# Optimization experiments

Hardware: AMD Instinct MI355X
Metric: run time of the kernel (lower is better)

Reference implementation:

```python
import jax, jax.numpy as jnp
import numpy as np

T = 12      # time_steps
N = 10000   # nodes per timestep graph
E = 160000  # edges per timestep graph
P = 30000   # node pairs
DIN = 128   # input_dim
H = 64      # hidden_dim
WND = 4     # attn_wnd


def setup_inputs() -> dict:
    key = jax.random.key(0)
    ks = jax.random.split(key, 12)
    x = jax.random.normal(ks[0], (2, T, N, DIN), dtype=jnp.float32)
    src = jax.random.randint(ks[1], (2, T, E), 0, N, dtype=jnp.int32)
    dst = jax.random.randint(ks[2], (2, T, E), 0, N, dtype=jnp.int32)
    idx = jax.random.randint(ks[3], (2, T, P), 0, N, dtype=jnp.int32)
    w_self = jax.random.normal(ks[4], (DIN, H), dtype=jnp.float32) * (1.0 / np.sqrt(DIN))
    w_neigh = jax.random.normal(ks[5], (DIN, H), dtype=jnp.float32) * (1.0 / np.sqrt(DIN))
    b_sage = jnp.zeros((H,), jnp.float32)
    w_ff2 = jax.random.normal(ks[6], (2 * H,), dtype=jnp.float32) * (1.0 / np.sqrt(2 * H))
    b_ff2 = jnp.zeros((), jnp.float32)
    w_ff1 = jax.random.normal(ks[7], (T,), dtype=jnp.float32) * (1.0 / np.sqrt(T))
    b_ff1 = jnp.zeros((), jnp.float32)
    w_out = jax.random.normal(ks[8], (2 * H, 1), dtype=jnp.float32) * (1.0 / np.sqrt(2 * H))
    return dict(x=x, src=src, dst=dst, idx=idx, w_self=w_self, w_neigh=w_neigh,
                b_sage=b_sage, w_ff2=w_ff2, b_ff2=b_ff2, w_ff1=w_ff1, b_ff1=b_ff1,
                w_out=w_out)


def _sage_all(x, src, dst, w_self, w_neigh, b_sage):
    """Mean-aggregation SAGEConv + L2 normalize, run over all 2*T graphs via scan."""
    xs = (x.reshape(2 * T, N, DIN), src.reshape(2 * T, E), dst.reshape(2 * T, E))

    def step(_, xe):
        xt, s, d = xe
        msum = jax.ops.segment_sum(xt[s], d, num_segments=N)            # [N, DIN]
        deg = jax.ops.segment_sum(jnp.ones((E,), xt.dtype), d, num_segments=N)
        mean = msum / jnp.maximum(deg, 1.0)[:, None]
        h = xt @ w_self + mean @ w_neigh + b_sage                       # [N, H]
        h = h / jnp.maximum(jnp.linalg.norm(h, axis=1, keepdims=True), 1e-12)
        return None, h

    _, hs = jax.lax.scan(step, None, xs)
    return hs.reshape(2, T, N, H)


def reference(x, src, dst, idx, w_self, w_neigh, b_sage, w_ff2, b_ff2, w_ff1, b_ff1, w_out):
    h = _sage_all(x, src, dst, w_self, w_neigh, b_sage)                 # [2, T, N, H]
    t_ar = jnp.arange(T)[:, None]
    hi = h[0][t_ar, idx[0]]                                             # [T, P, H]
    hj = h[1][t_ar, idx[1]]                                             # [T, P, H]
    temporal = jnp.concatenate([hi, hj], axis=-1).transpose(1, 0, 2)    # [P, T, 2H]

    def shifted(k):  # zero-pad shift along time by k
        return jnp.concatenate([jnp.zeros_like(temporal[:, :k]), temporal[:, :-k]], axis=1)

    # diff[k] = temporal - temporal shifted by (k+1) steps, k in [0, WND-2]
    diffs = jnp.stack([temporal - shifted(k + 1) for k in range(WND - 1)])  # [W-1, P, T, 2H]
    dw = jax.nn.relu(diffs @ w_ff2 + b_ff2)                              # [W-1, P, T]
    s = dw @ w_ff1 + b_ff1                                               # [W-1, P]
    sw = jax.nn.softmax(s, axis=0)[:, :, None, None]                     # softmax over window axis
    diff_att = jnp.sum(sw * jax.nn.sigmoid(diffs), axis=0)               # [P, T, 2H]
    outs = (temporal * diff_att).transpose(1, 0, 2)                      # [T, P, 2H]
    return (outs @ w_out)[..., 0]                                        # [T, P]
```

## Files before the change

kernel.cpp:

```cpp
#include <hip/hip_runtime.h>
#include <hip/hip_bf16.h>

#define TT 12
#define NNODE 10000
#define NEDGE 160000
#define NPAIR 30000
#define DIN 128
#define HH 64
#define NG 24
#define NROWS (NG * NNODE)
#define NEALL (NG * NEDGE)

typedef __attribute__((ext_vector_type(8))) short short8v;
typedef __attribute__((ext_vector_type(4))) float f32x4;

__device__ __forceinline__ short f2bf(float f) {
    unsigned u = __float_as_uint(f);
    unsigned r = u + 0x7fffu + ((u >> 16) & 1u);
    return (short)(r >> 16);
}
__device__ __forceinline__ float bf2f(short s) {
    return __uint_as_float(((unsigned)(unsigned short)s) << 16);
}

__global__ __launch_bounds__(256) void k_gemm_n(const float* __restrict__ x,
                                                const float* __restrict__ w,
                                                float* __restrict__ xn) {
    const int l = threadIdx.x & 63;
    const int wv = threadIdx.x >> 6;
    const int base = blockIdx.x * 64 + wv * 16;
    const int r15 = l & 15, q = l >> 4;
    f32x4 acc[4];
    #pragma unroll
    for (int c = 0; c < 4; ++c) acc[c] = (f32x4)0.f;
    #pragma unroll
    for (int s = 0; s < 4; ++s) {
        const float* xr = x + (size_t)(base + r15) * DIN + s * 32 + q * 8;
        float4 a0 = *(const float4*)xr;
        float4 a1 = *(const float4*)(xr + 4);
        float av[8] = {a0.x, a0.y, a0.z, a0.w, a1.x, a1.y, a1.z, a1.w};
        short8v ah, al;
        #pragma unroll
        for (int j = 0; j < 8; ++j) {
            short h = f2bf(av[j]); ah[j] = h; al[j] = f2bf(av[j] - bf2f(h));
        }
        #pragma unroll
        for (int c = 0; c < 4; ++c) {
            const float* wp = w + (size_t)(s * 32 + q * 8) * HH + c * 16 + r15;
            short8v bh, bl;
            #pragma unroll
            for (int j = 0; j < 8; ++j) {
                float v = wp[(size_t)j * HH];
                short h = f2bf(v); bh[j] = h; bl[j] = f2bf(v - bf2f(h));
            }
            acc[c] = __builtin_amdgcn_mfma_f32_16x16x32_bf16(ah, bh, acc[c], 0, 0, 0);
            acc[c] = __builtin_amdgcn_mfma_f32_16x16x32_bf16(ah, bl, acc[c], 0, 0, 0);
            acc[c] = __builtin_amdgcn_mfma_f32_16x16x32_bf16(al, bh, acc[c], 0, 0, 0);
        }
    }
    #pragma unroll
    for (int c = 0; c < 4; ++c)
        #pragma unroll
        for (int r = 0; r < 4; ++r)
            xn[(size_t)(base + q * 4 + r) * HH + c * 16 + r15] = acc[c][r];
}

__global__ __launch_bounds__(256) void k_gemm_sfin(const float* __restrict__ x,
                                                   const float* __restrict__ w,
                                                   const float* __restrict__ b_sage,
                                                   const float* __restrict__ msum,
                                                   float* __restrict__ hout) {
    const int l = threadIdx.x & 63;
    const int wv = threadIdx.x >> 6;
    const int base = blockIdx.x * 64 + wv * 16;
    const int r15 = l & 15, q = l >> 4;
    f32x4 acc[4];
    #pragma unroll
    for (int c = 0; c < 4; ++c) acc[c] = (f32x4)0.f;
    #pragma unroll
    for (int s = 0; s < 4; ++s) {
        const float* xr = x + (size_t)(base + r15) * DIN + s * 32 + q * 8;
        float4 a0 = *(const float4*)xr;
        float4 a1 = *(const float4*)(xr + 4);
        float av[8] = {a0.x, a0.y, a0.z, a0.w, a1.x, a1.y, a1.z, a1.w};
        short8v ah, al;
        #pragma unroll
        for (int j = 0; j < 8; ++j) {
            short h = f2bf(av[j]); ah[j] = h; al[j] = f2bf(av[j] - bf2f(h));
        }
        #pragma unroll
        for (int c = 0; c < 4; ++c) {
            const float* wp = w + (size_t)(s * 32 + q * 8) * HH + c * 16 + r15;
            short8v bh, bl;
            #pragma unroll
            for (int j = 0; j < 8; ++j) {
                float v = wp[(size_t)j * HH];
                short h = f2bf(v); bh[j] = h; bl[j] = f2bf(v - bf2f(h));
            }
            acc[c] = __builtin_amdgcn_mfma_f32_16x16x32_bf16(ah, bh, acc[c], 0, 0, 0);
            acc[c] = __builtin_amdgcn_mfma_f32_16x16x32_bf16(ah, bl, acc[c], 0, 0, 0);
            acc[c] = __builtin_amdgcn_mfma_f32_16x16x32_bf16(al, bh, acc[c], 0, 0, 0);
        }
    }
    float val[4][4];
    #pragma unroll
    for (int c = 0; c < 4; ++c) {
        int col = c * 16 + r15;
        float bb = b_sage[col];
        #pragma unroll
        for (int r = 0; r < 4; ++r) {
            int row = base + q * 4 + r;
            val[c][r] = acc[c][r] + bb + msum[(size_t)row * HH + col];
        }
    }
    #pragma unroll
    for (int r = 0; r < 4; ++r) {
        float ss = val[0][r] * val[0][r] + val[1][r] * val[1][r] +
                   val[2][r] * val[2][r] + val[3][r] * val[3][r];
        #pragma unroll
        for (int off = 1; off < 16; off <<= 1) ss += __shfl_xor(ss, off);
        float nrm = sqrtf(ss);
        nrm = nrm > 1e-12f ? nrm : 1e-12f;
        float inv = 1.f / nrm;
        #pragma unroll
        for (int c = 0; c < 4; ++c)
            hout[(size_t)(base + q * 4 + r) * HH + c * 16 + r15] = val[c][r] * inv;
    }
}

__global__ __launch_bounds__(256) void k_hist(const int* __restrict__ dst,
                                              int* __restrict__ deg_i) {
    int e = blockIdx.x * 256 + threadIdx.x;
    if (e >= NEALL) return;
    int g = e / NEDGE;
    atomicAdd(&deg_i[g * NNODE + dst[e]], 1);
}

__global__ __launch_bounds__(256) void k_scan(const int* __restrict__ deg_i,
                                              int* __restrict__ cursor) {
    const int g = blockIdx.x;
    const int t = threadIdx.x;
    const int base = g * NNODE;
    const int start = t * 40;
    const int cnt = start < NNODE ? (NNODE - start < 40 ? NNODE - start : 40) : 0;
    int s = 0;
    for (int i = 0; i < cnt; ++i) s += deg_i[base + start + i];
    __shared__ int sb[256];
    sb[t] = s;
    __syncthreads();
    #pragma unroll
    for (int d = 1; d < 256; d <<= 1) {
        int v = (t >= d) ? sb[t - d] : 0;
        __syncthreads();
        sb[t] += v;
        __syncthreads();
    }
    int run = sb[t] - s;
    for (int i = 0; i < cnt; ++i) {
        int d = deg_i[base + start + i];
        cursor[base + start + i] = run;
        run += d;
    }
}

__global__ __launch_bounds__(256) void k_fill(const int* __restrict__ src,
                                              const int* __restrict__ dst,
                                              int* __restrict__ cursor,
                                              int* __restrict__ csr) {
    int e = blockIdx.x * 256 + threadIdx.x;
    if (e >= NEALL) return;
    int g = e / NEDGE;
    int pos = atomicAdd(&cursor[g * NNODE + dst[e]], 1);
    csr[(size_t)g * NEDGE + pos] = src[e];
}

__global__ __launch_bounds__(256) void k_gath(const int* __restrict__ csr,
                                              const int* __restrict__ cursor,
                                              const int* __restrict__ deg_i,
                                              const float* __restrict__ xn,
                                              float* __restrict__ msum) {
    const int lane = threadIdx.x & 63;
    const int row = blockIdx.x * 4 + (threadIdx.x >> 6);
    if (row >= NROWS) return;
    const int g = row / NNODE;
    const int end = cursor[row];
    const int dg = deg_i[row];
    const int start = end - dg;
    const float* xg = xn + (size_t)g * NNODE * HH;
    const int* cs = csr + (size_t)g * NEDGE;
    float acc = 0.f;
    int j = start;
    for (; j + 4 <= end; j += 4) {
        int s0 = cs[j], s1 = cs[j + 1], s2 = cs[j + 2], s3 = cs[j + 3];
        float v0 = xg[(size_t)s0 * HH + lane];
        float v1 = xg[(size_t)s1 * HH + lane];
        float v2 = xg[(size_t)s2 * HH + lane];
        float v3 = xg[(size_t)s3 * HH + lane];
        acc += v0 + v1 + v2 + v3;
    }
    for (; j < end; ++j) acc += xg[(size_t)cs[j] * HH + lane];
    msum[(size_t)row * HH + lane] = (dg > 0) ? acc / (float)dg : 0.f;
}

__device__ __forceinline__ float sigmoidf_(float v) {
    return 1.0f / (1.0f + __expf(-v));
}

__global__ __launch_bounds__(256) void k_pair(const float* __restrict__ h,
                                              const int* __restrict__ idx,
                                              const float* __restrict__ w_ff2,
                                              const float* __restrict__ b_ff2p,
                                              const float* __restrict__ w_ff1,
                                              const float* __restrict__ b_ff1p,
                                              const float* __restrict__ w_out,
                                              float* __restrict__ out) {
    const int lane = threadIdx.x & 63;
    const int wave = threadIdx.x >> 6;
    const int p = blockIdx.x * 4 + wave;
    if (p >= NPAIR) return;
    const float wf2_0 = w_ff2[lane], wf2_1 = w_ff2[lane + 64];
    const float wo_0 = w_out[lane], wo_1 = w_out[lane + 64];
    const float bf2 = *b_ff2p, bf1 = *b_ff1p;

    float tv0[TT], tv1[TT], q[TT];
    #pragma unroll
    for (int t = 0; t < TT; ++t) {
        int i0 = idx[t * NPAIR + p];
        int i1 = idx[(TT + t) * NPAIR + p];
        tv0[t] = h[((size_t)t * NNODE + i0) * HH + lane];
        tv1[t] = h[((size_t)(TT + t) * NNODE + i1) * HH + lane];
        float part = tv0[t] * wf2_0 + tv1[t] * wf2_1;
        #pragma unroll
        for (int off = 32; off; off >>= 1) part += __shfl_xor(part, off);
        q[t] = part;
    }

    float s[3];
    #pragma unroll
    for (int k = 1; k <= 3; ++k) {
        float acc = bf1;
        #pragma unroll
        for (int t = 0; t < TT; ++t) {
            float dq = q[t] - (t >= k ? q[t - k] : 0.f);
            float r = dq + bf2;
            r = r > 0.f ? r : 0.f;
            acc += r * w_ff1[t];
        }
        s[k - 1] = acc;
    }
    float m = fmaxf(s[0], fmaxf(s[1], s[2]));
    float e0 = __expf(s[0] - m), e1 = __expf(s[1] - m), e2 = __expf(s[2] - m);
    float inv = 1.f / (e0 + e1 + e2);
    float sw0 = e0 * inv, sw1 = e1 * inv, sw2 = e2 * inv;

    #pragma unroll
    for (int t = 0; t < TT; ++t) {
        float a0, a1;
        {
            float d0 = tv0[t] - (t >= 1 ? tv0[t - 1] : 0.f);
            float d1 = tv1[t] - (t >= 1 ? tv1[t - 1] : 0.f);
            a0 = sw0 * sigmoidf_(d0);
            a1 = sw0 * sigmoidf_(d1);
        }
        {
            float d0 = tv0[t] - (t >= 2 ? tv0[t - 2] : 0.f);
            float d1 = tv1[t] - (t >= 2 ? tv1[t - 2] : 0.f);
            a0 += sw1 * sigmoidf_(d0);
            a1 += sw1 * sigmoidf_(d1);
        }
        {
            float d0 = tv0[t] - (t >= 3 ? tv0[t - 3] : 0.f);
            float d1 = tv1[t] - (t >= 3 ? tv1[t - 3] : 0.f);
            a0 += sw2 * sigmoidf_(d0);
            a1 += sw2 * sigmoidf_(d1);
        }
        float o = tv0[t] * a0 * wo_0 + tv1[t] * a1 * wo_1;
        #pragma unroll
        for (int off = 32; off; off >>= 1) o += __shfl_xor(o, off);
        if (lane == 0) out[t * NPAIR + p] = o;
    }
}

extern "C" void kernel_launch(void* const* d_in, const int* in_sizes, int n_in,
                              void* d_out, int out_size, void* d_ws, size_t ws_size,
                              hipStream_t stream) {
    const float* x      = (const float*)d_in[0];
    const int*   src    = (const int*)d_in[1];
    const int*   dst    = (const int*)d_in[2];
    const int*   idx    = (const int*)d_in[3];
    const float* w_self = (const float*)d_in[4];
    const float* w_neigh= (const float*)d_in[5];
    const float* b_sage = (const float*)d_in[6];
    const float* w_ff2  = (const float*)d_in[7];
    const float* b_ff2  = (const float*)d_in[8];
    const float* w_ff1  = (const float*)d_in[9];
    const float* b_ff1  = (const float*)d_in[10];
    const float* w_out  = (const float*)d_in[11];
    float* out = (float*)d_out;

    char* ws = (char*)d_ws;
    const size_t HB = (size_t)NROWS * HH * sizeof(float);
    const size_t NB = (size_t)NROWS * sizeof(int);
    float* xn_h  = (float*)ws;
    float* msum  = (float*)(ws + HB);
    int*   deg_i = (int*)(ws + 2 * HB);
    int*   cursor= (int*)(ws + 2 * HB + NB);
    int*   csr   = (int*)(ws + 2 * HB + 2 * NB);

    hipMemsetAsync(deg_i, 0, NB, stream);

    k_gemm_n<<<NROWS / 64, 256, 0, stream>>>(x, w_neigh, xn_h);
    k_hist<<<NEALL / 256, 256, 0, stream>>>(dst, deg_i);
    k_scan<<<NG, 256, 0, stream>>>(deg_i, cursor);
    k_fill<<<NEALL / 256, 256, 0, stream>>>(src, dst, cursor, csr);
    k_gath<<<NROWS / 4, 256, 0, stream>>>(csr, cursor, deg_i, xn_h, msum);
    k_gemm_sfin<<<NROWS / 64, 256, 0, stream>>>(x, w_self, b_sage, msum, xn_h);
    k_pair<<<NPAIR / 4, 256, 0, stream>>>(xn_h, idx, w_ff2, b_ff2, w_ff1, b_ff1,
                                          w_out, out);
}
```

Baseline: 874.0 us.

## Build CSR with node-range bucketed shared-memory atomics instead of global atomics

Result: slower. 1.197 ms (+36.9%).

```diff
diff --git a/kernel.cpp b/kernel.cpp
--- a/kernel.cpp
+++ b/kernel.cpp
@@ -10,6 +10,8 @@
 #define NG 24
 #define NROWS (NG * NNODE)
 #define NEALL (NG * NEDGE)
+#define NBUK 16
+#define BSZ (NNODE / NBUK)
 
 typedef __attribute__((ext_vector_type(8))) short short8v;
 typedef __attribute__((ext_vector_type(4))) float f32x4;
@@ -128,12 +130,21 @@
     }
 }
 
-__global__ __launch_bounds__(256) void k_hist(const int* __restrict__ dst,
-                                              int* __restrict__ deg_i) {
-    int e = blockIdx.x * 256 + threadIdx.x;
-    if (e >= NEALL) return;
-    int g = e / NEDGE;
-    atomicAdd(&deg_i[g * NNODE + dst[e]], 1);
+__global__ __launch_bounds__(256) void k_hist_b(const int* __restrict__ dst,
+                                                int* __restrict__ deg_i) {
+    __shared__ int cnt[BSZ];
+    const int g = blockIdx.y, b = blockIdx.x;
+    const int lo = b * BSZ;
+    for (int i = threadIdx.x; i < BSZ; i += 256) cnt[i] = 0;
+    __syncthreads();
+    const int* dg = dst + (size_t)g * NEDGE;
+    for (int e = threadIdx.x; e < NEDGE; e += 256) {
+        int d = dg[e] - lo;
+        if ((unsigned)d < (unsigned)BSZ) atomicAdd(&cnt[d], 1);
+    }
+    __syncthreads();
+    for (int i = threadIdx.x; i < BSZ; i += 256)
+        deg_i[g * NNODE + lo + i] = cnt[i];
 }
 
 __global__ __launch_bounds__(256) void k_scan(const int* __restrict__ deg_i,
@@ -163,15 +174,26 @@
     }
 }
 
-__global__ __launch_bounds__(256) void k_fill(const int* __restrict__ src,
-                                              const int* __restrict__ dst,
-                                              int* __restrict__ cursor,
-                                              int* __restrict__ csr) {
-    int e = blockIdx.x * 256 + threadIdx.x;
-    if (e >= NEALL) return;
-    int g = e / NEDGE;
-    int pos = atomicAdd(&cursor[g * NNODE + dst[e]], 1);
-    csr[(size_t)g * NEDGE + pos] = src[e];
+__global__ __launch_bounds__(256) void k_fill_b(const int* __restrict__ src,
+                                                const int* __restrict__ dst,
+                                                const int* __restrict__ cursor,
+                                                int* __restrict__ csr) {
+    __shared__ int cur[BSZ];
+    const int g = blockIdx.y, b = blockIdx.x;
+    const int lo = b * BSZ;
+    for (int i = threadIdx.x; i < BSZ; i += 256)
+        cur[i] = cursor[g * NNODE + lo + i];
+    __syncthreads();
+    const int* dg = dst + (size_t)g * NEDGE;
+    const int* sg = src + (size_t)g * NEDGE;
+    int* cs = csr + (size_t)g * NEDGE;
+    for (int e = threadIdx.x; e < NEDGE; e += 256) {
+        int d = dg[e] - lo;
+        if ((unsigned)d < (unsigned)BSZ) {
+            int pos = atomicAdd(&cur[d], 1);
+            cs[pos] = sg[e];
+        }
+    }
 }
 
 __global__ __launch_bounds__(256) void k_gath(const int* __restrict__ csr,
@@ -183,9 +205,9 @@
     const int row = blockIdx.x * 4 + (threadIdx.x >> 6);
     if (row >= NROWS) return;
     const int g = row / NNODE;
-    const int end = cursor[row];
+    const int start = cursor[row];
     const int dg = deg_i[row];
-    const int start = end - dg;
+    const int end = start + dg;
     const float* xg = xn + (size_t)g * NNODE * HH;
     const int* cs = csr + (size_t)g * NEDGE;
     float acc = 0.f;
@@ -307,12 +329,11 @@
     int*   cursor= (int*)(ws + 2 * HB + NB);
     int*   csr   = (int*)(ws + 2 * HB + 2 * NB);
 
-    hipMemsetAsync(deg_i, 0, NB, stream);
-
+    dim3 gbuk(NBUK, NG);
     k_gemm_n<<<NROWS / 64, 256, 0, stream>>>(x, w_neigh, xn_h);
-    k_hist<<<NEALL / 256, 256, 0, stream>>>(dst, deg_i);
+    k_hist_b<<<gbuk, 256, 0, stream>>>(dst, deg_i);
     k_scan<<<NG, 256, 0, stream>>>(deg_i, cursor);
-    k_fill<<<NEALL / 256, 256, 0, stream>>>(src, dst, cursor, csr);
+    k_fill_b<<<gbuk, 256, 0, stream>>>(src, dst, cursor, csr);
     k_gath<<<NROWS / 4, 256, 0, stream>>>(csr, cursor, deg_i, xn_h, msum);
     k_gemm_sfin<<<NROWS / 64, 256, 0, stream>>>(x, w_self, b_sage, msum, xn_h);
     k_pair<<<NPAIR / 4, 256, 0, stream>>>(xn_h, idx, w_ff2, b_ff2, w_ff1, b_ff1,
```

## Replace per-node CSR build with coarse bucket partition and LDS-atomic gather

Applied to the files above, without the earlier changes.

Measured after the change: 1.765 ms. +101.9%, slower.

```diff
diff --git a/kernel.cpp b/kernel.cpp
--- a/kernel.cpp
+++ b/kernel.cpp
@@ -9,7 +9,11 @@
 #define HH 64
 #define NG 24
 #define NROWS (NG * NNODE)
-#define NEALL (NG * NEDGE)
+#define NBUK 53
+#define BKN 192
+#define NCH 10
+#define ECH (NEDGE / NCH)
+#define SCN (NBUK * NCH)
 
 typedef __attribute__((ext_vector_type(8))) short short8v;
 typedef __attribute__((ext_vector_type(4))) float f32x4;
@@ -128,78 +132,115 @@
     }
 }
 
-__global__ __launch_bounds__(256) void k_hist(const int* __restrict__ dst,
-                                              int* __restrict__ deg_i) {
-    int e = blockIdx.x * 256 + threadIdx.x;
-    if (e >= NEALL) return;
-    int g = e / NEDGE;
-    atomicAdd(&deg_i[g * NNODE + dst[e]], 1);
-}
-
-__global__ __launch_bounds__(256) void k_scan(const int* __restrict__ deg_i,
-                                              int* __restrict__ cursor) {
-    const int g = blockIdx.x;
-    const int t = threadIdx.x;
-    const int base = g * NNODE;
-    const int start = t * 40;
-    const int cnt = start < NNODE ? (NNODE - start < 40 ? NNODE - start : 40) : 0;
+__global__ __launch_bounds__(256) void k_hcb(const int* __restrict__ dst,
+                                             int* __restrict__ hist) {
+    __shared__ int cnt[NBUK];
+    const int c = blockIdx.x, g = blockIdx.y;
+    for (int i = threadIdx.x; i < NBUK; i += 256) cnt[i] = 0;
+    __syncthreads();
+    const int* dg = dst + (size_t)g * NEDGE + c * ECH;
+    for (int e = threadIdx.x; e < ECH; e += 256)
+        atomicAdd(&cnt[dg[e] / BKN], 1);
+    __syncthreads();
+    for (int i = threadIdx.x; i < NBUK; i += 256)
+        hist[(g * NBUK + i) * NCH + c] = cnt[i];
+}
+
+__global__ __launch_bounds__(256) void k_scan2(const int* __restrict__ hist,
+                                               int* __restrict__ cbase) {
+    const int g = blockIdx.x, t = threadIdx.x;
+    const int* hg = hist + g * SCN;
+    int* cg = cbase + g * SCN;
+    int v[3];
     int s = 0;
-    for (int i = 0; i < cnt; ++i) s += deg_i[base + start + i];
+    #pragma unroll
+    for (int i = 0; i < 3; ++i) {
+        int ix = t * 3 + i;
+        v[i] = (ix < SCN) ? hg[ix] : 0;
+        s += v[i];
+    }
     __shared__ int sb[256];
     sb[t] = s;
     __syncthreads();
     #pragma unroll
     for (int d = 1; d < 256; d <<= 1) {
-        int v = (t >= d) ? sb[t - d] : 0;
+        int x = (t >= d) ? sb[t - d] : 0;
         __syncthreads();
-        sb[t] += v;
+        sb[t] += x;
         __syncthreads();
     }
     int run = sb[t] - s;
-    for (int i = 0; i < cnt; ++i) {
-        int d = deg_i[base + start + i];
-        cursor[base + start + i] = run;
-        run += d;
-    }
-}
-
-__global__ __launch_bounds__(256) void k_fill(const int* __restrict__ src,
+    #pragma unroll
+    for (int i = 0; i < 3; ++i) {
+        int ix = t * 3 + i;
+        if (ix < SCN) cg[ix] = run;
+        run += v[i];
+    }
+}
+
+__global__ __launch_bounds__(256) void k_part(const int* __restrict__ src,
                                               const int* __restrict__ dst,
-                                              int* __restrict__ cursor,
-                                              int* __restrict__ csr) {
-    int e = blockIdx.x * 256 + threadIdx.x;
-    if (e >= NEALL) return;
-    int g = e / NEDGE;
-    int pos = atomicAdd(&cursor[g * NNODE + dst[e]], 1);
-    csr[(size_t)g * NEDGE + pos] = src[e];
-}
-
-__global__ __launch_bounds__(256) void k_gath(const int* __restrict__ csr,
-                                              const int* __restrict__ cursor,
-                                              const int* __restrict__ deg_i,
-                                              const float* __restrict__ xn,
-                                              float* __restrict__ msum) {
-    const int lane = threadIdx.x & 63;
-    const int row = blockIdx.x * 4 + (threadIdx.x >> 6);
-    if (row >= NROWS) return;
-    const int g = row / NNODE;
-    const int end = cursor[row];
-    const int dg = deg_i[row];
-    const int start = end - dg;
+                                              const int* __restrict__ cbase,
+                                              int* __restrict__ packed) {
+    __shared__ int cur[NBUK];
+    const int c = blockIdx.x, g = blockIdx.y;
+    for (int i = threadIdx.x; i < NBUK; i += 256)
+        cur[i] = cbase[(g * NBUK + i) * NCH + c];
+    __syncthreads();
+    const size_t eo = (size_t)g * NEDGE + (size_t)c * ECH;
+    const int* dg = dst + eo;
+    const int* sg = src + eo;
+    int* pk = packed + (size_t)g * NEDGE;
+    for (int e = threadIdx.x; e < ECH; e += 256) {
+        int d = dg[e];
+        int b = d / BKN;
+        int pos = atomicAdd(&cur[b], 1);
+        pk[pos] = (sg[e] << 8) | (d - b * BKN);
+    }
+}
+
+__global__ __launch_bounds__(256) void k_pgath(const int* __restrict__ packed,
+                                               const int* __restrict__ cbase,
+                                               const float* __restrict__ xn,
+                                               float* __restrict__ msum) {
+    __shared__ float acc[BKN * HH];
+    __shared__ int degl[BKN];
+    const int b = blockIdx.x, g = blockIdx.y;
+    for (int i = threadIdx.x; i < BKN * HH; i += 256) acc[i] = 0.f;
+    for (int i = threadIdx.x; i < BKN; i += 256) degl[i] = 0;
+    __syncthreads();
+    const int start = cbase[(g * NBUK + b) * NCH];
+    const int end = (b == NBUK - 1) ? NEDGE : cbase[(g * NBUK + b + 1) * NCH];
+    const int lane = threadIdx.x & 63, wv = threadIdx.x >> 6;
+    const int* pk = packed + (size_t)g * NEDGE;
     const float* xg = xn + (size_t)g * NNODE * HH;
-    const int* cs = csr + (size_t)g * NEDGE;
-    float acc = 0.f;
-    int j = start;
-    for (; j + 4 <= end; j += 4) {
-        int s0 = cs[j], s1 = cs[j + 1], s2 = cs[j + 2], s3 = cs[j + 3];
-        float v0 = xg[(size_t)s0 * HH + lane];
-        float v1 = xg[(size_t)s1 * HH + lane];
-        float v2 = xg[(size_t)s2 * HH + lane];
-        float v3 = xg[(size_t)s3 * HH + lane];
-        acc += v0 + v1 + v2 + v3;
-    }
-    for (; j < end; ++j) acc += xg[(size_t)cs[j] * HH + lane];
-    msum[(size_t)row * HH + lane] = (dg > 0) ? acc / (float)dg : 0.f;
+    int e = start + wv;
+    for (; e + 4 < end; e += 8) {
+        int p0 = pk[e], p1 = pk[e + 4];
+        float v0 = xg[(size_t)(p0 >> 8) * HH + lane];
+        float v1 = xg[(size_t)(p1 >> 8) * HH + lane];
+        atomicAdd(&acc[(p0 & 255) * HH + lane], v0);
+        atomicAdd(&acc[(p1 & 255) * HH + lane], v1);
+        if (lane == 0) {
+            atomicAdd(&degl[p0 & 255], 1);
+            atomicAdd(&degl[p1 & 255], 1);
+        }
+    }
+    for (; e < end; e += 4) {
+        int p = pk[e];
+        float v = xg[(size_t)(p >> 8) * HH + lane];
+        atomicAdd(&acc[(p & 255) * HH + lane], v);
+        if (lane == 0) atomicAdd(&degl[p & 255], 1);
+    }
+    __syncthreads();
+    const int gbase = b * BKN;
+    for (int n = wv; n < BKN; n += 4) {
+        int gn = gbase + n;
+        if (gn >= NNODE) break;
+        float dgv = (float)degl[n];
+        if (dgv < 1.f) dgv = 1.f;
+        msum[((size_t)g * NNODE + gn) * HH + lane] = acc[n * HH + lane] / dgv;
+    }
 }
 
 __device__ __forceinline__ float sigmoidf_(float v) {
@@ -300,20 +341,21 @@
 
     char* ws = (char*)d_ws;
     const size_t HB = (size_t)NROWS * HH * sizeof(float);
-    const size_t NB = (size_t)NROWS * sizeof(int);
+    const size_t SB = (size_t)NG * SCN * sizeof(int);
     float* xn_h  = (float*)ws;
     float* msum  = (float*)(ws + HB);
-    int*   deg_i = (int*)(ws + 2 * HB);
-    int*   cursor= (int*)(ws + 2 * HB + NB);
-    int*   csr   = (int*)(ws + 2 * HB + 2 * NB);
-
-    hipMemsetAsync(deg_i, 0, NB, stream);
-
+    int*   hist  = (int*)(ws + 2 * HB);
+    int*   cbase = (int*)(ws + 2 * HB + 51200);
+    int*   packed= (int*)(ws + 2 * HB + 2 * 51200);
+    (void)SB;
+
+    dim3 gcg(NCH, NG);
+    dim3 gbg(NBUK, NG);
     k_gemm_n<<<NROWS / 64, 256, 0, stream>>>(x, w_neigh, xn_h);
-    k_hist<<<NEALL / 256, 256, 0, stream>>>(dst, deg_i);
-    k_scan<<<NG, 256, 0, stream>>>(deg_i, cursor);
-    k_fill<<<NEALL / 256, 256, 0, stream>>>(src, dst, cursor, csr);
-    k_gath<<<NROWS / 4, 256, 0, stream>>>(csr, cursor, deg_i, xn_h, msum);
+    k_hcb<<<gcg, 256, 0, stream>>>(dst, hist);
+    k_scan2<<<NG, 256, 0, stream>>>(hist, cbase);
+    k_part<<<gcg, 256, 0, stream>>>(src, dst, cbase, packed);
+    k_pgath<<<gbg, 256, 0, stream>>>(packed, cbase, xn_h, msum);
     k_gemm_sfin<<<NROWS / 64, 256, 0, stream>>>(x, w_self, b_sage, msum, xn_h);
     k_pair<<<NPAIR / 4, 256, 0, stream>>>(xn_h, idx, w_ff2, b_ff2, w_ff1, b_ff1,
                                           w_out, out);
```
